# Optimization experiments

Hardware: AMD Instinct MI355X
Metric: run time of the kernel (lower is better)

Reference implementation:

```python
import jax, jax.numpy as jnp
import numpy as np

TOP_K = 30
NUM_RBF = 16
EDGE_F = 128
NODE_F = 128
MAXREL = 32
EDGE_IN = NUM_RBF * 25  # 400


def _normalize(x, eps=1e-12):
    n = jnp.linalg.norm(x, axis=-1, keepdims=True)
    return x / jnp.maximum(n, eps)


def _rbf(D):
    # D: [..., ] distances -> [..., NUM_RBF]
    mu = jnp.linspace(2.0, 22.0, NUM_RBF)
    sigma = (22.0 - 2.0) / NUM_RBF
    return jnp.exp(-(((D[..., None] - mu) / sigma) ** 2))


def _layer_norm(x, g, b, eps=1e-5):
    m = x.mean(-1, keepdims=True)
    v = ((x - m) ** 2).mean(-1, keepdims=True)
    return (x - m) / jnp.sqrt(v + eps) * g + b


def setup_inputs() -> dict:
    key = jax.random.key(0)
    ks = jax.random.split(key, 8)
    B, L = 8, 1024
    X = jax.random.normal(ks[0], (B, L, 5, 3), jnp.float32) * 3.0  # backbone coords
    mask = jnp.ones((B, L), jnp.float32)
    Lvec = jnp.full((B,), L, dtype=jnp.int32)
    W_edge = jax.random.normal(ks[1], (EDGE_IN, EDGE_F), jnp.float32) * 0.05
    W_node = jax.random.normal(ks[2], (6, NODE_F), jnp.float32) * 0.05
    W_pos = jax.random.normal(ks[3], (2 * MAXREL + 1, EDGE_F), jnp.float32) * 0.05
    b_pos = jnp.zeros((EDGE_F,), jnp.float32)
    g_edge = jnp.ones((EDGE_F,), jnp.float32)
    b_edge = jnp.zeros((EDGE_F,), jnp.float32)
    g_node = jnp.ones((NODE_F,), jnp.float32)
    b_node = jnp.zeros((NODE_F,), jnp.float32)
    return {"X": X, "mask": mask, "Lvec": Lvec, "W_edge": W_edge, "W_node": W_node,
            "W_pos": W_pos, "b_pos": b_pos, "g_edge": g_edge, "b_edge": b_edge,
            "g_node": g_node, "b_node": b_node}


def reference(X, mask, Lvec, W_edge, W_node, W_pos, b_pos, g_edge, b_edge, g_node, b_node):
    B, L = X.shape[0], X.shape[1]
    N, Ca, C, CB, O = (X[:, :, i, :] for i in range(5))

    # backbone frames (4x4: rotation rows e1,e2,e3; translation Ca; bottom row zeros)
    v1 = C - Ca
    v2 = N - Ca
    e1 = _normalize(v1)
    u2 = v2 - e1 * jnp.sum(e1 * v2, axis=-1, keepdims=True)
    e2 = _normalize(u2)
    e3 = jnp.cross(e1, e2)
    R = jnp.stack([e1, e2, e3], axis=-2)  # [B,L,3,3]
    bb = jnp.zeros((B, L, 4, 4), X.dtype).at[..., :3, :3].set(R).at[..., :3, 3].set(Ca)

    # _dist: masked Ca-Ca pairwise distance + kNN
    mask2 = mask[:, None, :] * mask[:, :, None]  # [B,L,L]
    dX = Ca[:, :, None, :] - Ca[:, None, :, :]
    D = mask2 * jnp.sqrt(jnp.sum(dX ** 2, -1) + 1e-6)
    D_max = jnp.max(D, -1, keepdims=True)
    D_adjust = D + (1.0 - mask2) * D_max
    k = min(TOP_K, L)
    negD, E_idx = jax.lax.top_k(-D_adjust, k)  # smallest-k distances
    D_neighbors = -negD  # [B,L,K]

    # RBFs: compute distances only at selected neighbors (same math as full cdist+gather)
    bidx = jnp.arange(B)[:, None, None]

    def get_rbf(A, Bc):
        Bnb = Bc[bidx, E_idx]  # [B,L,K,3]
        d = jnp.sqrt(jnp.sum((A[:, :, None, :] - Bnb) ** 2, -1) + 1e-6)
        return _rbf(d)

    pairs = [(N, N), (C, C), (O, O), (CB, CB), (Ca, N), (Ca, C), (Ca, O), (Ca, CB),
             (N, C), (N, O), (N, CB), (CB, C), (CB, O), (O, C), (N, Ca), (C, Ca),
             (O, Ca), (CB, Ca), (C, N), (O, N), (CB, N), (C, CB), (O, CB), (C, O)]
    RBF_all = jnp.concatenate([_rbf(D_neighbors)] + [get_rbf(a, b) for a, b in pairs], axis=-1)  # [B,L,K,400]

    # positional encodings over sequence offsets of selected neighbors
    offset = jnp.arange(L)[None, :, None] - E_idx  # residue_idx[i] - residue_idx[j]
    d_clip = jnp.clip(offset + MAXREL, 0, 2 * MAXREL)
    E_pos = jax.nn.one_hot(d_clip, 2 * MAXREL + 1, dtype=X.dtype) @ W_pos + b_pos

    # dihedrals (phi, psi, omega) from N/CA/C chain
    X3 = X[:, :, :3, :].reshape(B, 3 * L, 3)
    dXc = X3[:, 1:, :] - X3[:, :-1, :]
    U = _normalize(dXc)
    u_2, u_1, u_0 = U[:, :-2, :], U[:, 1:-1, :], U[:, 2:, :]
    n_2 = _normalize(jnp.cross(u_2, u_1))
    n_1 = _normalize(jnp.cross(u_1, u_0))
    cosD = jnp.clip(jnp.sum(n_2 * n_1, -1), -1 + 1e-7, 1 - 1e-7)
    Dang = jnp.sign(jnp.sum(u_2 * n_1, -1)) * jnp.arccos(cosD)
    Dang = jnp.pad(Dang, ((0, 0), (1, 2))).reshape(B, L, 3)
    V = jnp.concatenate([jnp.cos(Dang), jnp.sin(Dang)], -1)  # [B,L,6]

    E = _layer_norm(RBF_all @ W_edge + E_pos, g_edge, b_edge)
    V = _layer_norm(V @ W_node, g_node, b_node)
    return (V, E, E_idx, bb)
```

## Files before the change

### kernel.cpp

```cpp
#include <hip/hip_runtime.h>
#include <hip/hip_bf16.h>
#include <math.h>

#define V_OFF    ((size_t)0)
#define E_OFF    ((size_t)1048576)
#define EIDX_OFF ((size_t)32505856)
#define BB_OFF   ((size_t)32751616)

#define K 30
#define NRBF 16
#define AH   232
#define SSTR 132

typedef __attribute__((ext_vector_type(8))) short bf16x8;
typedef __attribute__((ext_vector_type(4))) float f32x4;

__device__ __constant__ int c_pairA[24] = {0,2,4,3,1,1,1,1,0,0,0,3,3,4,0,2,4,3,2,4,3,2,4,2};
__device__ __constant__ int c_pairB[24] = {0,2,4,3,0,2,4,3,2,4,3,2,4,2,1,1,1,1,0,0,0,3,3,4};

__device__ __constant__ float c_muS[16] = {
    1.92179871f, 3.20299785f, 4.48419699f, 5.76539613f, 7.04659527f, 8.32779441f,
    9.60899355f, 10.89019269f, 12.17139183f, 13.45259097f, 14.73379011f, 16.01498925f,
    17.29618839f, 18.57738753f, 19.85858667f, 21.13978581f};

__device__ __forceinline__ unsigned short f2bu(float f) {
    unsigned x = __float_as_uint(f);
    return (unsigned short)((x + 0x7fffu + ((x >> 16) & 1u)) >> 16);
}

__device__ __forceinline__ unsigned wave_umin64(unsigned x) {
    unsigned t;
    t = __builtin_amdgcn_update_dpp(x, x, 0x111, 0xf, 0xf, false); x = min(x, t);
    t = __builtin_amdgcn_update_dpp(x, x, 0x112, 0xf, 0xf, false); x = min(x, t);
    t = __builtin_amdgcn_update_dpp(x, x, 0x114, 0xf, 0xf, false); x = min(x, t);
    t = __builtin_amdgcn_update_dpp(x, x, 0x118, 0xf, 0xf, false); x = min(x, t);
    t = __builtin_amdgcn_update_dpp(x, x, 0x142, 0xf, 0xf, false); x = min(x, t);
    t = __builtin_amdgcn_update_dpp(x, x, 0x143, 0xf, 0xf, false); x = min(x, t);
    return (unsigned)__builtin_amdgcn_readlane((int)x, 63);
}
__device__ __forceinline__ unsigned wave_umax64(unsigned x) {
    unsigned t;
    t = __builtin_amdgcn_update_dpp(x, x, 0x111, 0xf, 0xf, false); x = max(x, t);
    t = __builtin_amdgcn_update_dpp(x, x, 0x112, 0xf, 0xf, false); x = max(x, t);
    t = __builtin_amdgcn_update_dpp(x, x, 0x114, 0xf, 0xf, false); x = max(x, t);
    t = __builtin_amdgcn_update_dpp(x, x, 0x118, 0xf, 0xf, false); x = max(x, t);
    t = __builtin_amdgcn_update_dpp(x, x, 0x142, 0xf, 0xf, false); x = max(x, t);
    t = __builtin_amdgcn_update_dpp(x, x, 0x143, 0xf, 0xf, false); x = max(x, t);
    return (unsigned)__builtin_amdgcn_readlane((int)x, 63);
}
#define U64_STEP(ctl) { \
    const unsigned lo_ = (unsigned)x, hi_ = (unsigned)(x >> 32); \
    const unsigned plo = __builtin_amdgcn_update_dpp(lo_, lo_, ctl, 0xf, 0xf, false); \
    const unsigned phi = __builtin_amdgcn_update_dpp(hi_, hi_, ctl, 0xf, 0xf, false); \
    const unsigned long long p = ((unsigned long long)phi << 32) | plo; \
    x = p < x ? p : x; }
__device__ __forceinline__ unsigned long long wave_u64min(unsigned long long x) {
    U64_STEP(0x111) U64_STEP(0x112) U64_STEP(0x114)
    U64_STEP(0x118) U64_STEP(0x142) U64_STEP(0x143)
    const unsigned rlo = (unsigned)__builtin_amdgcn_readlane((int)(unsigned)x, 63);
    const unsigned rhi = (unsigned)__builtin_amdgcn_readlane((int)(unsigned)(x >> 32), 63);
    return ((unsigned long long)rhi << 32) | rlo;
}
__device__ __forceinline__ unsigned mbcnt64(unsigned long long m) {
    return __builtin_amdgcn_mbcnt_hi((unsigned)(m >> 32),
           __builtin_amdgcn_mbcnt_lo((unsigned)m, 0u));
}
__device__ __forceinline__ float group8_fadd(float x) {
    float t;
    t = __int_as_float(__builtin_amdgcn_update_dpp(__float_as_int(x), __float_as_int(x), 0x0B1, 0xf, 0xf, false)); x += t;
    t = __int_as_float(__builtin_amdgcn_update_dpp(__float_as_int(x), __float_as_int(x), 0x04E, 0xf, 0xf, false)); x += t;
    x += __shfl_xor(x, 4, 64);
    return x;
}

__device__ __forceinline__ void norm_to(const float v[3], float o[3]) {
    float n = sqrtf(v[0]*v[0] + v[1]*v[1] + v[2]*v[2]);
    n = fmaxf(n, 1e-12f);
    o[0] = v[0]/n; o[1] = v[1]/n; o[2] = v[2]/n;
}
__device__ __forceinline__ void unit_diff(const float a[3], const float b[3], float o[3]) {
    float v[3] = {a[0]-b[0], a[1]-b[1], a[2]-b[2]};
    norm_to(v, o);
}
__device__ __forceinline__ void cross_unit(const float a[3], const float b[3], float o[3]) {
    float c[3] = {a[1]*b[2]-a[2]*b[1], a[2]*b[0]-a[0]*b[2], a[0]*b[1]-a[1]*b[0]};
    norm_to(c, o);
}

__global__ __launch_bounds__(128) void wb_prep_kernel(
    const float* __restrict__ We, unsigned short* __restrict__ Wb)
{
    const int s = blockIdx.x;
    const int j = threadIdx.x;
    unsigned* dst = (unsigned*)(Wb + ((size_t)(s*128 + j) << 5));
    #pragma unroll
    for (int m = 0; m < 16; ++m) {
        const int k0 = s*32 + 2*m;
        const unsigned lo = (k0   < 400) ? f2bu(We[(size_t)k0*128 + j])     : 0u;
        const unsigned hi = (k0+1 < 400) ? f2bu(We[(size_t)(k0+1)*128 + j]) : 0u;
        dst[m] = (hi << 16) | lo;
    }
}

__global__ __launch_bounds__(256) void rbf_tab_kernel(unsigned* __restrict__ tab)
{
    const int idx = blockIdx.x*256 + threadIdx.x;
    const float t1 = (idx * 0.02f) * 0.96089935f;
    unsigned* dst = tab + ((size_t)idx << 3);
    #pragma unroll
    for (int m = 0; m < 8; ++m) {
        const float z0 = t1 - c_muS[2*m];
        const float z1 = t1 - c_muS[2*m+1];
        const float v0 = exp2f(-z0*z0);
        const float v1 = exp2f(-z1*z1);
        unsigned pk;
        asm("v_cvt_pk_bf16_f32 %0, %1, %2" : "=v"(pk) : "v"(v0), "v"(v1));
        dst[m] = pk;
    }
}

__global__ __launch_bounds__(128) void node_bb_kernel(
    const float* __restrict__ X, const float* __restrict__ Wn,
    const float* __restrict__ gn, const float* __restrict__ bn,
    float* __restrict__ out, float4* __restrict__ ca4)
{
    const int blk = blockIdx.x;
    const int b = blk >> 10, i = blk & 1023;
    const int tid = threadIdx.x;
    __shared__ float ang[3];
    __shared__ float red[128];

    if (tid < 3) {
        const int m = 3*i + tid;
        float dang = 0.f;
        if (m >= 1 && m <= 3*1024 - 3) {
            const int t = m - 1;
            float P[4][3];
            #pragma unroll
            for (int q = 0; q < 4; ++q) {
                const int s = t + q;
                const int ri = s / 3, ai = s - 3*ri;
                const float* p = X + (((size_t)b * 1024 + ri) * 5 + ai) * 3;
                P[q][0] = p[0]; P[q][1] = p[1]; P[q][2] = p[2];
            }
            float u2v[3], u1v[3], u0v[3];
            unit_diff(P[1], P[0], u2v);
            unit_diff(P[2], P[1], u1v);
            unit_diff(P[3], P[2], u0v);
            float n2v[3], n1v[3];
            cross_unit(u2v, u1v, n2v);
            cross_unit(u1v, u0v, n1v);
            float cosD = n2v[0]*n1v[0] + n2v[1]*n1v[1] + n2v[2]*n1v[2];
            cosD = fminf(fmaxf(cosD, -1.f + 1e-7f), 1.f - 1e-7f);
            float sg = u2v[0]*n1v[0] + u2v[1]*n1v[1] + u2v[2]*n1v[2];
            float s = (sg > 0.f) ? 1.f : ((sg < 0.f) ? -1.f : 0.f);
            dang = s * acosf(cosD);
        }
        ang[tid] = dang;
    }
    if (tid == 3) {
        const float* p = X + (size_t)blk * 15;
        float Nx=p[0],  Ny=p[1],  Nz=p[2];
        float Cax=p[3], Cay=p[4], Caz=p[5];
        float Cx=p[6],  Cy=p[7],  Cz=p[8];
        ca4[blk] = make_float4(Cax, Cay, Caz, 0.f);
        float v1[3] = {Cx-Cax, Cy-Cay, Cz-Caz};
        float v2[3] = {Nx-Cax, Ny-Cay, Nz-Caz};
        float e1[3]; norm_to(v1, e1);
        float dd = e1[0]*v2[0] + e1[1]*v2[1] + e1[2]*v2[2];
        float u2[3] = {v2[0]-e1[0]*dd, v2[1]-e1[1]*dd, v2[2]-e1[2]*dd};
        float e2[3]; norm_to(u2, e2);
        float e3[3] = {e1[1]*e2[2]-e1[2]*e2[1], e1[2]*e2[0]-e1[0]*e2[2], e1[0]*e2[1]-e1[1]*e2[0]};
        float* bb = out + BB_OFF + (size_t)blk * 16;
        bb[0]=e1[0]; bb[1]=e1[1]; bb[2]=e1[2];  bb[3]=Cax;
        bb[4]=e2[0]; bb[5]=e2[1]; bb[6]=e2[2];  bb[7]=Cay;
        bb[8]=e3[0]; bb[9]=e3[1]; bb[10]=e3[2]; bb[11]=Caz;
        bb[12]=0.f; bb[13]=0.f; bb[14]=0.f; bb[15]=0.f;
    }
    __syncthreads();
    const float a0 = ang[0], a1 = ang[1], a2 = ang[2];
    float feat[6] = {cosf(a0), cosf(a1), cosf(a2), sinf(a0), sinf(a1), sinf(a2)};
    float x = 0.f;
    #pragma unroll
    for (int f = 0; f < 6; ++f) x += feat[f] * Wn[f*128 + tid];
    red[tid] = x; __syncthreads();
    for (int s = 64; s > 0; s >>= 1) { if (tid < s) red[tid] += red[tid+s]; __syncthreads(); }
    const float mean = red[0] * (1.f/128.f);
    __syncthreads();
    const float xm = x - mean;
    red[tid] = xm*xm; __syncthreads();
    for (int s = 64; s > 0; s >>= 1) { if (tid < s) red[tid] += red[tid+s]; __syncthreads(); }
    const float var = red[0] * (1.f/128.f);
    const float y = xm / __fsqrt_rn(var + 1e-5f) * gn[tid] + bn[tid];
    out[V_OFF + (size_t)blk * 128 + tid] = y;
}

__global__ __launch_bounds__(256, 8) void topk_edge_kernel(
    const float* __restrict__ X, const float* __restrict__ mask,
    const unsigned short* __restrict__ Wb, const float* __restrict__ Wp,
    const float* __restrict__ bp, const float* __restrict__ ge,
    const float* __restrict__ be, const float4* __restrict__ ca4,
    const unsigned* __restrict__ rtab, float* __restrict__ out)
{
    const int blk = blockIdx.x;
    const int b = blk >> 10, i = blk & 1023;
    const int tid = threadIdx.x;
    const int w = tid >> 6, lane = tid & 63;

    __shared__ __align__(16) unsigned char uni_raw[K * SSTR * 4];
    __shared__ float redf4[4];
    __shared__ unsigned redT[4];
    __shared__ int   scount;
    __shared__ float nbA[K][15];
    __shared__ int   nj[K];
    __shared__ float dnbv[K];
    unsigned short* A_lds = (unsigned short*)uni_raw;
    float* S = (float*)uni_raw;
    unsigned long long* surv = (unsigned long long*)uni_raw;

    if (tid == 0) scount = 0;

    const float4 me = ca4[(b << 10) + i];
    const float mi  = mask[(b << 10) + i];

    float dv_r[4], m2_r[4];
    float lmax = -1.f;
    #pragma unroll
    for (int m = 0; m < 4; ++m) {
        const int j = tid + (m << 8);
        const float4 cj = ca4[(b << 10) + j];
        const float dx = __fsub_rn(me.x, cj.x);
        const float dy = __fsub_rn(me.y, cj.y);
        const float dz = __fsub_rn(me.z, cj.z);
        const float ss = __fadd_rn(__fadd_rn(__fmul_rn(dx,dx), __fmul_rn(dy,dy)), __fmul_rn(dz,dz));
        const float dist = __fsqrt_rn(__fadd_rn(ss, 1e-6f));
        const float m2 = __fmul_rn(mi, mask[(b << 10) + j]);
        const float Dv = __fmul_rn(m2, dist);
        dv_r[m] = Dv; m2_r[m] = m2;
        lmax = fmaxf(lmax, Dv);
    }
    const float wmax = __uint_as_float(wave_umax64(__float_as_uint(lmax)));
    if (lane == 0) redf4[w] = wmax;
    __syncthreads();
    const float Dmax = fmaxf(fmaxf(redf4[0], redf4[1]), fmaxf(redf4[2], redf4[3]));

    unsigned va[4];
    #pragma unroll
    for (int m = 0; m < 4; ++m)
        va[m] = __float_as_uint(__fadd_rn(dv_r[m], __fmul_rn(__fsub_rn(1.f, m2_r[m]), Dmax)));

    {
        unsigned vb0 = va[0], vb1 = va[1], vb2 = va[2], vb3 = va[3];
        unsigned v = 0;
        #pragma unroll
        for (int k = 0; k < 8; ++k) {
            const unsigned head = min(min(vb0, vb1), min(vb2, vb3));
            v = wave_umin64(head);
            vb0 = (vb0 == v) ? 0xffffffffu : vb0;
            vb1 = (vb1 == v) ? 0xffffffffu : vb1;
            vb2 = (vb2 == v) ? 0xffffffffu : vb2;
            vb3 = (vb3 == v) ? 0xffffffffu : vb3;
        }
        if (lane == 0) redT[w] = v;
    }
    __syncthreads();
    const unsigned T = max(max(redT[0], redT[1]), max(redT[2], redT[3]));

    {
        unsigned long long mm0 = __ballot(va[0] <= T);
        unsigned long long mm1 = __ballot(va[1] <= T);
        unsigned long long mm2 = __ballot(va[2] <= T);
        unsigned long long mm3 = __ballot(va[3] <= T);
        const unsigned c0 = __popcll(mm0), c1 = __popcll(mm1);
        const unsigned c2 = __popcll(mm2), c3 = __popcll(mm3);
        int old = 0;
        if (lane == 0) old = atomicAdd(&scount, (int)(c0 + c1 + c2 + c3));
        unsigned base = (unsigned)__builtin_amdgcn_readfirstlane(old);
        if (va[0] <= T) surv[base + mbcnt64(mm0)] = ((unsigned long long)va[0] << 32) | (unsigned)tid;
        base += c0;
        if (va[1] <= T) surv[base + mbcnt64(mm1)] = ((unsigned long long)va[1] << 32) | (unsigned)(tid + 256);
        base += c1;
        if (va[2] <= T) surv[base + mbcnt64(mm2)] = ((unsigned long long)va[2] << 32) | (unsigned)(tid + 512);
        base += c2;
        if (va[3] <= T) surv[base + mbcnt64(mm3)] = ((unsigned long long)va[3] << 32) | (unsigned)(tid + 768);
    }
    __syncthreads();
    const int N = scount;

    if (w == 0) {
        if (N <= 128) {
            unsigned long long k0 = (lane < N) ? surv[lane] : ~0ull;
            unsigned long long k1 = (lane + 64 < N) ? surv[lane + 64] : ~0ull;
            for (int k = 0; k < K; ++k) {
                const unsigned long long h = k0 < k1 ? k0 : k1;
                const unsigned long long best = wave_u64min(h);
                k0 = (k0 == best) ? ~0ull : k0;
                k1 = (k1 == best) ? ~0ull : k1;
                if (lane == 0) {
                    const int j = (int)(best & 0xffffffffu);
                    nj[k] = j;
                    dnbv[k] = __uint_as_float((unsigned)(best >> 32));
                    out[EIDX_OFF + (size_t)blk * K + k] = (float)j;
                }
            }
        } else {
            for (int k = 0; k < K; ++k) {
                unsigned long long h = ~0ull;
                for (int t = lane; t < N; t += 64) { const unsigned long long c = surv[t]; h = c < h ? c : h; }
                const unsigned long long best = wave_u64min(h);
                for (int t = lane; t < N; t += 64) if (surv[t] == best) surv[t] = ~0ull;
                if (lane == 0) {
                    const int j = (int)(best & 0xffffffffu);
                    nj[k] = j;
                    dnbv[k] = __uint_as_float((unsigned)(best >> 32));
                    out[EIDX_OFF + (size_t)blk * K + k] = (float)j;
                }
            }
        }
    }
    __syncthreads();

    for (int t = tid; t < K*15; t += 256) {
        const int e = t / 15, r = t - e*15;
        nbA[e][r] = X[((size_t)(b << 10) + nj[e])*15 + r];
    }
    __syncthreads();

    const float* sa = X + (size_t)blk * 15;
    f32x4 acc00 = {0,0,0,0}, acc01 = {0,0,0,0}, acc10 = {0,0,0,0}, acc11 = {0,0,0,0};
    const int ar = lane & 15;
    const int kg = (lane >> 4) * 8;
    const unsigned short* a_base = A_lds + ar*AH + kg;
    const unsigned short* a_base1 = a_base + 16*AH;
    const unsigned short* b_base = Wb + ((size_t)(w*32 + ar) << 5) + kg;

    for (int t = tid; t < K*12; t += 256) {
        const int e = t / 12, g = t - e*12;
        float d;
        if (g == 0) d = dnbv[e];
        else {
            const int p = g - 1;
            const int aA = c_pairA[p], aB = c_pairB[p];
            const float dx = sa[aA*3+0] - nbA[e][aB*3+0];
            const float dy = sa[aA*3+1] - nbA[e][aB*3+1];
            const float dz = sa[aA*3+2] - nbA[e][aB*3+2];
            d = sqrtf(dx*dx + dy*dy + dz*dz + 1e-6f);
        }
        int idx = (int)__fmaf_rn(d, 50.f, 0.5f);
        idx = min(idx, 4095);
        const uint4* src = (const uint4*)(rtab + ((size_t)idx << 3));
        uint4* dst = (uint4*)(A_lds + e*AH + g*NRBF);
        dst[0] = src[0]; dst[1] = src[1];
    }
    __syncthreads();
    #pragma unroll
    for (int s = 0; s < 6; ++s) {
        const bf16x8 a0 = *reinterpret_cast<const bf16x8*>(a_base + s*32);
        const bf16x8 a1 = *reinterpret_cast<const bf16x8*>(a_base1 + s*32);
        const bf16x8 b0 = *reinterpret_cast<const bf16x8*>(b_base + (size_t)s*4096);
        const bf16x8 b1 = *reinterpret_cast<const bf16x8*>(b_base + (size_t)s*4096 + 512);
        acc00 = __builtin_amdgcn_mfma_f32_16x16x32_bf16(a0, b0, acc00, 0, 0, 0);
        acc01 = __builtin_amdgcn_mfma_f32_16x16x32_bf16(a0, b1, acc01, 0, 0, 0);
        acc10 = __builtin_amdgcn_mfma_f32_16x16x32_bf16(a1, b0, acc10, 0, 0, 0);
        acc11 = __builtin_amdgcn_mfma_f32_16x16x32_bf16(a1, b1, acc11, 0, 0, 0);
    }
    __syncthreads();

    for (int t = tid; t < K*13; t += 256) {
        const int e = t / 13, gg = t - e*13;
        const int p = 11 + gg;
        const int aA = c_pairA[p], aB = c_pairB[p];
        const float dx = sa[aA*3+0] - nbA[e][aB*3+0];
        const float dy = sa[aA*3+1] - nbA[e][aB*3+1];
        const float dz = sa[aA*3+2] - nbA[e][aB*3+2];
        const float d = sqrtf(dx*dx + dy*dy + dz*dz + 1e-6f);
        int idx = (int)__fmaf_rn(d, 50.f, 0.5f);
        idx = min(idx, 4095);
        const uint4* src = (const uint4*)(rtab + ((size_t)idx << 3));
        uint4* dst = (uint4*)(A_lds + e*AH + gg*NRBF);
        dst[0] = src[0]; dst[1] = src[1];
    }
    for (int t = tid; t < K*8; t += 256) {
        const int e = t >> 3, c = t & 7;
        ((unsigned*)(A_lds + e*AH + 208))[c] = 0u;
    }
    __syncthreads();
    #pragma unroll
    for (int s = 0; s < 7; ++s) {
        const bf16x8 a0 = *reinterpret_cast<const bf16x8*>(a_base + s*32);
        const bf16x8 a1 = *reinterpret_cast<const bf16x8*>(a_base1 + s*32);
        const bf16x8 b0 = *reinterpret_cast<const bf16x8*>(b_base + (size_t)(6+s)*4096);
        const bf16x8 b1 = *reinterpret_cast<const bf16x8*>(b_base + (size_t)(6+s)*4096 + 512);
        acc00 = __builtin_amdgcn_mfma_f32_16x16x32_bf16(a0, b0, acc00, 0, 0, 0);
        acc01 = __builtin_amdgcn_mfma_f32_16x16x32_bf16(a0, b1, acc01, 0, 0, 0);
        acc10 = __builtin_amdgcn_mfma_f32_16x16x32_bf16(a1, b0, acc10, 0, 0, 0);
        acc11 = __builtin_amdgcn_mfma_f32_16x16x32_bf16(a1, b1, acc11, 0, 0, 0);
    }
    __syncthreads();

    {
        const int crow = (lane >> 4) * 4;
        const int ccol = w*32 + (lane & 15);
        #pragma unroll
        for (int r = 0; r < 4; ++r) {
            const int r0 = crow + r;
            if (r0 < K) { S[r0*SSTR + ccol] = acc00[r]; S[r0*SSTR + ccol + 16] = acc01[r]; }
            const int r1 = 16 + crow + r;
            if (r1 < K) { S[r1*SSTR + ccol] = acc10[r]; S[r1*SSTR + ccol + 16] = acc11[r]; }
        }
    }
    __syncthreads();

    #pragma unroll
    for (int n = 0; n < 4; ++n) {
        const int item = tid + (n << 8);
        if (item < 960) {
            const int e = item >> 5, q = item & 31;
            int off = i - nj[e] + 32;
            off = off < 0 ? 0 : (off > 64 ? 64 : off);
            const float4 wp = ((const float4*)(Wp + (size_t)off*128))[q];
            const float4 bq = ((const float4*)bp)[q];
            float4* sp = (float4*)(S + e*SSTR) + q;
            float4 sv = *sp;
            sv.x += wp.x + bq.x; sv.y += wp.y + bq.y;
            sv.z += wp.z + bq.z; sv.w += wp.w + bq.w;
            *sp = sv;
        }
    }
    __syncthreads();

    {
        const int e = tid >> 3, s8 = tid & 7;
        if (e < K) {
            const float* row = S + e*SSTR + s8*16;
            float xv[16];
            float sum = 0.f;
            #pragma unroll
            for (int c = 0; c < 4; ++c) {
                const float4 q = ((const float4*)row)[c];
                xv[4*c+0] = q.x; xv[4*c+1] = q.y; xv[4*c+2] = q.z; xv[4*c+3] = q.w;
                sum += q.x + q.y + q.z + q.w;
            }
            const float mean = group8_fadd(sum) * (1.f/128.f);
            float vs = 0.f;
            #pragma unroll
            for (int c = 0; c < 16; ++c) { const float d = xv[c] - mean; xv[c] = d; vs = __fmaf_rn(d, d, vs); }
            const float inv = 1.f / __fsqrt_rn(group8_fadd(vs) * (1.f/128.f) + 1e-5f);
            const int j0 = s8*16;
            float* op = out + E_OFF + ((size_t)blk * K + e) * 128 + j0;
            #pragma unroll
            for (int c = 0; c < 4; ++c) {
                const float4 g4 = ((const float4*)(ge + j0))[c];
                const float4 b4 = ((const float4*)(be + j0))[c];
                float4 o;
                o.x = xv[4*c+0] * inv * g4.x + b4.x;
                o.y = xv[4*c+1] * inv * g4.y + b4.y;
                o.z = xv[4*c+2] * inv * g4.z + b4.z;
                o.w = xv[4*c+3] * inv * g4.w + b4.w;
                ((float4*)op)[c] = o;
            }
        }
    }
}

extern "C" void kernel_launch(void* const* d_in, const int* in_sizes, int n_in,
                              void* d_out, int out_size, void* d_ws, size_t ws_size,
                              hipStream_t stream) {
    const float* X    = (const float*)d_in[0];
    const float* mask = (const float*)d_in[1];
    const float* We   = (const float*)d_in[3];
    const float* Wn   = (const float*)d_in[4];
    const float* Wp   = (const float*)d_in[5];
    const float* bp   = (const float*)d_in[6];
    const float* gE   = (const float*)d_in[7];
    const float* bE   = (const float*)d_in[8];
    const float* gN   = (const float*)d_in[9];
    const float* bN   = (const float*)d_in[10];
    float* out = (float*)d_out;
    unsigned short* Wb = (unsigned short*)d_ws;
    float4* ca4 = (float4*)((char*)d_ws + 106496);
    unsigned* rtab = (unsigned*)((char*)d_ws + 106496 + 131072);

    hipLaunchKernelGGL(wb_prep_kernel,   dim3(13),   dim3(128), 0, stream, We, Wb);
    hipLaunchKernelGGL(rbf_tab_kernel,   dim3(16),   dim3(256), 0, stream, rtab);
    hipLaunchKernelGGL(node_bb_kernel,   dim3(8192), dim3(128), 0, stream, X, Wn, gN, bN, out, ca4);
    hipLaunchKernelGGL(topk_edge_kernel, dim3(8192), dim3(256), 0, stream,
                       X, mask, Wb, Wp, bp, gE, bE, ca4, rtab, out);
}
```

Before: 157.8 us.

## Fuse node features into top-k kernel and use parallel rank-based selection

The separate node/backbone-frame kernel, which launched 8192 blocks of 128 threads, is removed. Its dihedral, frame and node layer-norm work now runs at the tail of topk_edge_kernel, with wave-level DPP reductions in place of the shared-memory tree. A tiny ca_pack kernel now only packs the Ca coordinates. The serial single-wave 30-step min-extraction top-k is replaced by every thread counting its survivor's rank in parallel. This removes a launch and the serial selection latency, at the cost of O(N^2) LDS reads per block and a barrier that is executed by only some of the waves.

Measured after the change: 139.2 us. 1.13x faster.

```diff
diff --git a/kernel.cpp b/kernel.cpp
--- a/kernel.cpp
+++ b/kernel.cpp
@@ -48,18 +48,15 @@
     t = __builtin_amdgcn_update_dpp(x, x, 0x143, 0xf, 0xf, false); x = max(x, t);
     return (unsigned)__builtin_amdgcn_readlane((int)x, 63);
 }
-#define U64_STEP(ctl) { \
-    const unsigned lo_ = (unsigned)x, hi_ = (unsigned)(x >> 32); \
-    const unsigned plo = __builtin_amdgcn_update_dpp(lo_, lo_, ctl, 0xf, 0xf, false); \
-    const unsigned phi = __builtin_amdgcn_update_dpp(hi_, hi_, ctl, 0xf, 0xf, false); \
-    const unsigned long long p = ((unsigned long long)phi << 32) | plo; \
-    x = p < x ? p : x; }
-__device__ __forceinline__ unsigned long long wave_u64min(unsigned long long x) {
-    U64_STEP(0x111) U64_STEP(0x112) U64_STEP(0x114)
-    U64_STEP(0x118) U64_STEP(0x142) U64_STEP(0x143)
-    const unsigned rlo = (unsigned)__builtin_amdgcn_readlane((int)(unsigned)x, 63);
-    const unsigned rhi = (unsigned)__builtin_amdgcn_readlane((int)(unsigned)(x >> 32), 63);
-    return ((unsigned long long)rhi << 32) | rlo;
+__device__ __forceinline__ float wave_fadd64(float x) {
+    float t;
+    t = __int_as_float(__builtin_amdgcn_update_dpp(0, __float_as_int(x), 0x111, 0xf, 0xf, true)); x += t;
+    t = __int_as_float(__builtin_amdgcn_update_dpp(0, __float_as_int(x), 0x112, 0xf, 0xf, true)); x += t;
+    t = __int_as_float(__builtin_amdgcn_update_dpp(0, __float_as_int(x), 0x114, 0xf, 0xf, true)); x += t;
+    t = __int_as_float(__builtin_amdgcn_update_dpp(0, __float_as_int(x), 0x118, 0xf, 0xf, true)); x += t;
+    t = __int_as_float(__builtin_amdgcn_update_dpp(0, __float_as_int(x), 0x142, 0xf, 0xf, true)); x += t;
+    t = __int_as_float(__builtin_amdgcn_update_dpp(0, __float_as_int(x), 0x143, 0xf, 0xf, true)); x += t;
+    return __int_as_float(__builtin_amdgcn_readlane(__float_as_int(x), 63));
 }
 __device__ __forceinline__ unsigned mbcnt64(unsigned long long m) {
     return __builtin_amdgcn_mbcnt_hi((unsigned)(m >> 32),
@@ -119,80 +116,12 @@
     }
 }
 
-__global__ __launch_bounds__(128) void node_bb_kernel(
-    const float* __restrict__ X, const float* __restrict__ Wn,
-    const float* __restrict__ gn, const float* __restrict__ bn,
-    float* __restrict__ out, float4* __restrict__ ca4)
+__global__ __launch_bounds__(256) void ca_pack_kernel(
+    const float* __restrict__ X, float4* __restrict__ ca4)
 {
-    const int blk = blockIdx.x;
-    const int b = blk >> 10, i = blk & 1023;
-    const int tid = threadIdx.x;
-    __shared__ float ang[3];
-    __shared__ float red[128];
-
-    if (tid < 3) {
-        const int m = 3*i + tid;
-        float dang = 0.f;
-        if (m >= 1 && m <= 3*1024 - 3) {
-            const int t = m - 1;
-            float P[4][3];
-            #pragma unroll
-            for (int q = 0; q < 4; ++q) {
-                const int s = t + q;
-                const int ri = s / 3, ai = s - 3*ri;
-                const float* p = X + (((size_t)b * 1024 + ri) * 5 + ai) * 3;
-                P[q][0] = p[0]; P[q][1] = p[1]; P[q][2] = p[2];
-            }
-            float u2v[3], u1v[3], u0v[3];
-            unit_diff(P[1], P[0], u2v);
-            unit_diff(P[2], P[1], u1v);
-            unit_diff(P[3], P[2], u0v);
-            float n2v[3], n1v[3];
-            cross_unit(u2v, u1v, n2v);
-            cross_unit(u1v, u0v, n1v);
-            float cosD = n2v[0]*n1v[0] + n2v[1]*n1v[1] + n2v[2]*n1v[2];
-            cosD = fminf(fmaxf(cosD, -1.f + 1e-7f), 1.f - 1e-7f);
-            float sg = u2v[0]*n1v[0] + u2v[1]*n1v[1] + u2v[2]*n1v[2];
-            float s = (sg > 0.f) ? 1.f : ((sg < 0.f) ? -1.f : 0.f);
-            dang = s * acosf(cosD);
-        }
-        ang[tid] = dang;
-    }
-    if (tid == 3) {
-        const float* p = X + (size_t)blk * 15;
-        float Nx=p[0],  Ny=p[1],  Nz=p[2];
-        float Cax=p[3], Cay=p[4], Caz=p[5];
-        float Cx=p[6],  Cy=p[7],  Cz=p[8];
-        ca4[blk] = make_float4(Cax, Cay, Caz, 0.f);
-        float v1[3] = {Cx-Cax, Cy-Cay, Cz-Caz};
-        float v2[3] = {Nx-Cax, Ny-Cay, Nz-Caz};
-        float e1[3]; norm_to(v1, e1);
-        float dd = e1[0]*v2[0] + e1[1]*v2[1] + e1[2]*v2[2];
-        float u2[3] = {v2[0]-e1[0]*dd, v2[1]-e1[1]*dd, v2[2]-e1[2]*dd};
-        float e2[3]; norm_to(u2, e2);
-        float e3[3] = {e1[1]*e2[2]-e1[2]*e2[1], e1[2]*e2[0]-e1[0]*e2[2], e1[0]*e2[1]-e1[1]*e2[0]};
-        float* bb = out + BB_OFF + (size_t)blk * 16;
-        bb[0]=e1[0]; bb[1]=e1[1]; bb[2]=e1[2];  bb[3]=Cax;
-        bb[4]=e2[0]; bb[5]=e2[1]; bb[6]=e2[2];  bb[7]=Cay;
-        bb[8]=e3[0]; bb[9]=e3[1]; bb[10]=e3[2]; bb[11]=Caz;
-        bb[12]=0.f; bb[13]=0.f; bb[14]=0.f; bb[15]=0.f;
-    }
-    __syncthreads();
-    const float a0 = ang[0], a1 = ang[1], a2 = ang[2];
-    float feat[6] = {cosf(a0), cosf(a1), cosf(a2), sinf(a0), sinf(a1), sinf(a2)};
-    float x = 0.f;
-    #pragma unroll
-    for (int f = 0; f < 6; ++f) x += feat[f] * Wn[f*128 + tid];
-    red[tid] = x; __syncthreads();
-    for (int s = 64; s > 0; s >>= 1) { if (tid < s) red[tid] += red[tid+s]; __syncthreads(); }
-    const float mean = red[0] * (1.f/128.f);
-    __syncthreads();
-    const float xm = x - mean;
-    red[tid] = xm*xm; __syncthreads();
-    for (int s = 64; s > 0; s >>= 1) { if (tid < s) red[tid] += red[tid+s]; __syncthreads(); }
-    const float var = red[0] * (1.f/128.f);
-    const float y = xm / __fsqrt_rn(var + 1e-5f) * gn[tid] + bn[tid];
-    out[V_OFF + (size_t)blk * 128 + tid] = y;
+    const int idx = blockIdx.x*256 + threadIdx.x;
+    const float* p = X + (size_t)idx*15;
+    ca4[idx] = make_float4(p[3], p[4], p[5], 0.f);
 }
 
 __global__ __launch_bounds__(256, 8) void topk_edge_kernel(
@@ -200,7 +129,9 @@
     const unsigned short* __restrict__ Wb, const float* __restrict__ Wp,
     const float* __restrict__ bp, const float* __restrict__ ge,
     const float* __restrict__ be, const float4* __restrict__ ca4,
-    const unsigned* __restrict__ rtab, float* __restrict__ out)
+    const unsigned* __restrict__ rtab,
+    const float* __restrict__ Wn, const float* __restrict__ gn,
+    const float* __restrict__ bn, float* __restrict__ out)
 {
     const int blk = blockIdx.x;
     const int b = blk >> 10, i = blk & 1023;
@@ -214,6 +145,7 @@
     __shared__ float nbA[K][15];
     __shared__ int   nj[K];
     __shared__ float dnbv[K];
+    __shared__ float angf[3];
     unsigned short* A_lds = (unsigned short*)uni_raw;
     float* S = (float*)uni_raw;
     unsigned long long* surv = (unsigned long long*)uni_raw;
@@ -287,34 +219,18 @@
     __syncthreads();
     const int N = scount;
 
-    if (w == 0) {
-        if (N <= 128) {
-            unsigned long long k0 = (lane < N) ? surv[lane] : ~0ull;
-            unsigned long long k1 = (lane + 64 < N) ? surv[lane + 64] : ~0ull;
-            for (int k = 0; k < K; ++k) {
-                const unsigned long long h = k0 < k1 ? k0 : k1;
-                const unsigned long long best = wave_u64min(h);
-                k0 = (k0 == best) ? ~0ull : k0;
-                k1 = (k1 == best) ? ~0ull : k1;
-                if (lane == 0) {
-                    const int j = (int)(best & 0xffffffffu);
-                    nj[k] = j;
-                    dnbv[k] = __uint_as_float((unsigned)(best >> 32));
-                    out[EIDX_OFF + (size_t)blk * K + k] = (float)j;
-                }
-            }
-        } else {
-            for (int k = 0; k < K; ++k) {
-                unsigned long long h = ~0ull;
-                for (int t = lane; t < N; t += 64) { const unsigned long long c = surv[t]; h = c < h ? c : h; }
-                const unsigned long long best = wave_u64min(h);
-                for (int t = lane; t < N; t += 64) if (surv[t] == best) surv[t] = ~0ull;
-                if (lane == 0) {
-                    const int j = (int)(best & 0xffffffffu);
-                    nj[k] = j;
-                    dnbv[k] = __uint_as_float((unsigned)(best >> 32));
-                    out[EIDX_OFF + (size_t)blk * K + k] = (float)j;
-                }
+    for (int base = 0; base < N; base += 256) {
+        const int t = base + tid;
+        if (t < N) {
+            const unsigned long long mykey = surv[t];
+            int rank = 0;
+            #pragma unroll 4
+            for (int u = 0; u < N; ++u) rank += (surv[u] < mykey) ? 1 : 0;
+            if (rank < K) {
+                const int j = (int)(mykey & 0xffffffffu);
+                nj[rank] = j;
+                dnbv[rank] = __uint_as_float((unsigned)(mykey >> 32));
+                out[EIDX_OFF + (size_t)blk * K + rank] = (float)j;
             }
         }
     }
@@ -461,6 +377,72 @@
             }
         }
     }
+
+    if (tid < 3) {
+        const int m = 3*i + tid;
+        float dang = 0.f;
+        if (m >= 1 && m <= 3*1024 - 3) {
+            const int t = m - 1;
+            float P[4][3];
+            #pragma unroll
+            for (int q = 0; q < 4; ++q) {
+                const int s = t + q;
+                const int ri = s / 3, ai = s - 3*ri;
+                const float* p = X + (((size_t)b * 1024 + ri) * 5 + ai) * 3;
+                P[q][0] = p[0]; P[q][1] = p[1]; P[q][2] = p[2];
+            }
+            float u2v[3], u1v[3], u0v[3];
+            unit_diff(P[1], P[0], u2v);
+            unit_diff(P[2], P[1], u1v);
+            unit_diff(P[3], P[2], u0v);
+            float n2v[3], n1v[3];
+            cross_unit(u2v, u1v, n2v);
+            cross_unit(u1v, u0v, n1v);
+            float cosD = n2v[0]*n1v[0] + n2v[1]*n1v[1] + n2v[2]*n1v[2];
+            cosD = fminf(fmaxf(cosD, -1.f + 1e-7f), 1.f - 1e-7f);
+            float sg = u2v[0]*n1v[0] + u2v[1]*n1v[1] + u2v[2]*n1v[2];
+            float s = (sg > 0.f) ? 1.f : ((sg < 0.f) ? -1.f : 0.f);
+            dang = s * acosf(cosD);
+        }
+        angf[tid] = dang;
+    }
+    if (tid == 3) {
+        float Nx=sa[0],  Ny=sa[1],  Nz=sa[2];
+        float Cax=sa[3], Cay=sa[4], Caz=sa[5];
+        float Cx=sa[6],  Cy=sa[7],  Cz=sa[8];
+        float v1[3] = {Cx-Cax, Cy-Cay, Cz-Caz};
+        float v2[3] = {Nx-Cax, Ny-Cay, Nz-Caz};
+        float e1[3]; norm_to(v1, e1);
+        float dd = e1[0]*v2[0] + e1[1]*v2[1] + e1[2]*v2[2];
+        float u2[3] = {v2[0]-e1[0]*dd, v2[1]-e1[1]*dd, v2[2]-e1[2]*dd};
+        float e2[3]; norm_to(u2, e2);
+        float e3[3] = {e1[1]*e2[2]-e1[2]*e2[1], e1[2]*e2[0]-e1[0]*e2[2], e1[0]*e2[1]-e1[1]*e2[0]};
+        float* bb = out + BB_OFF + (size_t)blk * 16;
+        bb[0]=e1[0]; bb[1]=e1[1]; bb[2]=e1[2];  bb[3]=Cax;
+        bb[4]=e2[0]; bb[5]=e2[1]; bb[6]=e2[2];  bb[7]=Cay;
+        bb[8]=e3[0]; bb[9]=e3[1]; bb[10]=e3[2]; bb[11]=Caz;
+        bb[12]=0.f; bb[13]=0.f; bb[14]=0.f; bb[15]=0.f;
+    }
+    __syncthreads();
+    float xV = 0.f;
+    if (tid < 128) {
+        const float a0 = angf[0], a1 = angf[1], a2 = angf[2];
+        const float feat[6] = {cosf(a0), cosf(a1), cosf(a2), sinf(a0), sinf(a1), sinf(a2)};
+        #pragma unroll
+        for (int f = 0; f < 6; ++f) xV += feat[f] * Wn[f*128 + tid];
+        const float s = wave_fadd64(xV);
+        if (lane == 0) redf4[w] = s;
+    }
+    __syncthreads();
+    if (tid < 128) {
+        const float mean = (redf4[0] + redf4[1]) * (1.f/128.f);
+        const float xm = xV - mean;
+        const float vsum = wave_fadd64(xm*xm);
+        if (lane == 0) redT[w] = __float_as_uint(vsum);
+        __builtin_amdgcn_s_barrier();
+        const float var = (__uint_as_float(redT[0]) + __uint_as_float(redT[1])) * (1.f/128.f);
+        out[V_OFF + (size_t)blk * 128 + tid] = xm / __fsqrt_rn(var + 1e-5f) * gn[tid] + bn[tid];
+    }
 }
 
 extern "C" void kernel_launch(void* const* d_in, const int* in_sizes, int n_in,
@@ -483,7 +465,7 @@
 
     hipLaunchKernelGGL(wb_prep_kernel,   dim3(13),   dim3(128), 0, stream, We, Wb);
     hipLaunchKernelGGL(rbf_tab_kernel,   dim3(16),   dim3(256), 0, stream, rtab);
-    hipLaunchKernelGGL(node_bb_kernel,   dim3(8192), dim3(128), 0, stream, X, Wn, gN, bN, out, ca4);
+    hipLaunchKernelGGL(ca_pack_kernel,   dim3(32),   dim3(256), 0, stream, X, ca4);
     hipLaunchKernelGGL(topk_edge_kernel, dim3(8192), dim3(256), 0, stream,
-                       X, mask, Wb, Wp, bp, gE, bE, ca4, rtab, out);
-}
+                       X, mask, Wb, Wp, bp, gE, bE, ca4, rtab, Wn, gN, bN, out);
+}
```
